# Kernel tuning notes

Hardware: AMD Instinct MI355X
Metric: run time of the kernel (lower is better)

## Reference

```python
import jax, jax.numpy as jnp
import numpy as np

H = 8          # num_heads
NEG = -1e30    # masked-score value
EPS = 1e-5


def layer_norm(h, g, b):
    mu = jnp.mean(h, -1, keepdims=True)
    v = jnp.mean(jnp.square(h - mu), -1, keepdims=True)
    return (h - mu) * jax.lax.rsqrt(v + EPS) * g + b


def mha(q_in, kv_in, in_w, in_b, out_w, out_b, mask):
    # in_w: [3D, D] packed q/k/v projections (PyTorch MultiheadAttention layout)
    D = q_in.shape[-1]
    dh = D // H
    wq, wk, wv = in_w[:D], in_w[D:2 * D], in_w[2 * D:]
    bq, bk, bv = in_b[:D], in_b[D:2 * D], in_b[2 * D:]
    q = (q_in @ wq.T + bq).reshape(q_in.shape[0], q_in.shape[1], H, dh)
    k = (kv_in @ wk.T + bk).reshape(kv_in.shape[0], kv_in.shape[1], H, dh)
    v = (kv_in @ wv.T + bv).reshape(kv_in.shape[0], kv_in.shape[1], H, dh)
    s = jnp.einsum('bqhd,bkhd->bhqk', q, k) / jnp.sqrt(jnp.float32(dh))
    if mask is not None:
        s = s + mask  # [1,1,S,S] additive causal mask
    a = jax.nn.softmax(s, axis=-1)
    o = jnp.einsum('bhqk,bkhd->bqhd', a, v).reshape(q_in.shape[0], q_in.shape[1], D)
    return o @ out_w.T + out_b


def _forward(x, start_query, one_emb, zero_emb,
             sa_in_w, sa_in_b, sa_out_w, sa_out_b,
             ca_in_w, ca_in_b, ca_out_w, ca_out_b,
             lin1_w, lin1_b, lin2_w, lin2_b,
             ln_g, ln_b, cls_w, cls_b, label):
    B, S, D = x.shape
    n = label.shape[0]  # == S
    # Teacher-forced decoder inputs: [start_query, emb(label[0]), ..., emb(label[n-2])]
    tok = jnp.where((label[:-1] > 0.5)[:, None], one_emb[None, :], zero_emb[None, :])  # [n-1, D]
    tgt = jnp.concatenate([start_query[None, :], tok], axis=0)  # [n, D]
    h = jnp.broadcast_to(tgt[None], (B, n, D))
    causal = jnp.tril(jnp.ones((n, n), dtype=bool))
    mask = jnp.where(causal, 0.0, NEG).astype(x.dtype)[None, None]
    L = sa_in_w.shape[0]
    for l in range(L):
        # post-LN TransformerDecoderLayer (PyTorch default, relu FFN)
        sa = mha(h, h, sa_in_w[l], sa_in_b[l], sa_out_w[l], sa_out_b[l], mask)
        h = layer_norm(h + sa, ln_g[l, 0], ln_b[l, 0])
        ca = mha(h, x, ca_in_w[l], ca_in_b[l], ca_out_w[l], ca_out_b[l], None)
        h = layer_norm(h + ca, ln_g[l, 1], ln_b[l, 1])
        ff = jax.nn.relu(h @ lin1_w[l].T + lin1_b[l]) @ lin2_w[l].T + lin2_b[l]
        h = layer_norm(h + ff, ln_g[l, 2], ln_b[l, 2])
    # classifier + sigmoid; output[b, i] == decoder(tf[:1+i])[-1] of the original loop
    return jax.nn.sigmoid(h @ cls_w.T + cls_b)  # [B, n, 1]


def setup_inputs() -> dict:
    key = jax.random.key(0)
    ks = iter(jax.random.split(key, 32))
    B, S, D, FF, L = 8, 1024, 1024, 2048, 6

    def w(shape, s=0.02):
        return jax.random.normal(next(ks), shape, jnp.float32) * s

    return dict(
        x=jax.random.normal(next(ks), (B, S, D), jnp.float32),
        label=jax.random.uniform(next(ks), (S,), jnp.float32),
        start_query=jax.random.uniform(next(ks), (D,), jnp.float32),
        one_emb=jax.random.uniform(next(ks), (D,), jnp.float32),
        zero_emb=jax.random.uniform(next(ks), (D,), jnp.float32),
        sa_in_w=w((L, 3 * D, D)), sa_in_b=jnp.zeros((L, 3 * D), jnp.float32),
        sa_out_w=w((L, D, D)), sa_out_b=jnp.zeros((L, D), jnp.float32),
        ca_in_w=w((L, 3 * D, D)), ca_in_b=jnp.zeros((L, 3 * D), jnp.float32),
        ca_out_w=w((L, D, D)), ca_out_b=jnp.zeros((L, D), jnp.float32),
        lin1_w=w((L, FF, D)), lin1_b=jnp.zeros((L, FF), jnp.float32),
        lin2_w=w((L, D, FF)), lin2_b=jnp.zeros((L, D), jnp.float32),
        ln_g=jnp.ones((L, 3, D), jnp.float32), ln_b=jnp.zeros((L, 3, D), jnp.float32),
        cls_w=w((1, D)), cls_b=jnp.zeros((1,), jnp.float32),
    )


def reference(x, label, start_query, one_emb, zero_emb,
              sa_in_w, sa_in_b, sa_out_w, sa_out_b,
              ca_in_w, ca_in_b, ca_out_w, ca_out_b,
              lin1_w, lin1_b, lin2_w, lin2_b,
              ln_g, ln_b, cls_w, cls_b):
    return _forward(x, start_query, one_emb, zero_emb,
                    sa_in_w, sa_in_b, sa_out_w, sa_out_b,
                    ca_in_w, ca_in_b, ca_out_w, ca_out_b,
                    lin1_w, lin1_b, lin2_w, lin2_b,
                    ln_g, ln_b, cls_w, cls_b, label)
```

## Files before the change

### kernel.cpp

```cpp
#include <hip/hip_runtime.h>
#include <stdint.h>

typedef __attribute__((ext_vector_type(8))) short short8;
typedef __attribute__((ext_vector_type(4))) float f32x4;
typedef __attribute__((ext_vector_type(4))) float float4v;
typedef __attribute__((ext_vector_type(4))) unsigned short ushort4v;

__device__ __forceinline__ float b2f(short u) {
  union { float f; uint32_t i; } v; v.i = ((uint32_t)(unsigned short)u) << 16; return v.f;
}
__device__ __forceinline__ short f2b(float f) {
  uint32_t x = __float_as_uint(f);
  uint32_t r = (x + 0x7fffu + ((x >> 16) & 1u)) >> 16;
  return (short)r;
}
__device__ __forceinline__ void gload16(const short* g, short* l) {
  __builtin_amdgcn_global_load_lds((__attribute__((address_space(1))) const void*)g,
                                   (__attribute__((address_space(3))) void*)l, 16, 0, 0);
}

__global__ void f2b_kernel(const float* __restrict__ in, short* __restrict__ out, int n4) {
  int i = blockIdx.x * blockDim.x + threadIdx.x;
  int stride = gridDim.x * blockDim.x;
  for (; i < n4; i += stride) {
    float4v v = *((const float4v*)in + i);
    ushort4v o;
    o[0] = (unsigned short)f2b(v[0]); o[1] = (unsigned short)f2b(v[1]);
    o[2] = (unsigned short)f2b(v[2]); o[3] = (unsigned short)f2b(v[3]);
    *((ushort4v*)out + i) = o;
  }
}

__global__ void h0_kernel(const float* __restrict__ label, const float* __restrict__ sq,
                          const float* __restrict__ onee, const float* __restrict__ zeroe,
                          short* __restrict__ h) {
  int i = blockIdx.x;
  const float* src = (i == 0) ? sq : (label[i - 1] > 0.5f ? onee : zeroe);
  int d = threadIdx.x * 4;
  float4v v = *(const float4v*)(src + d);
  ushort4v o;
  o[0] = (unsigned short)f2b(v[0]); o[1] = (unsigned short)f2b(v[1]);
  o[2] = (unsigned short)f2b(v[2]); o[3] = (unsigned short)f2b(v[3]);
#pragma unroll
  for (int b = 0; b < 8; ++b)
    *(ushort4v*)(h + ((size_t)b * 1024 + i) * 1024 + d) = o;
}

__device__ __forceinline__ void stage_grp(const short* __restrict__ mat, size_t rc0,
                                          int K, int kt, short* dstbuf, int w, int lane, int g2) {
  const int w3 = w & 3;
  const int rlo = lane >> 3;
  const int us = (lane & 7) ^ rlo;
#pragma unroll
  for (int q = 0; q < 4; ++q) {
    int c;
    if (w < 4) c = g2 * 8 + w3 * 2 + (q & 1) + (q >> 1) * 16;
    else       c = g2 * 4 + w3 + (q & 1) * 8 + (q >> 1) * 16;
    int rih = (c & 15) * 8 + rlo;
    gload16(mat + (rc0 + (c >> 4) * 128 + rih) * (size_t)K + kt * 64 + us * 8,
            dstbuf + ((w >> 2) * 32 + c) * 512);
  }
}

template <int EPI>
__global__ __launch_bounds__(512, 2) void gemm256(const short* __restrict__ A,
                                                  const short* __restrict__ W,
                                                  const float* __restrict__ bias,
                                                  short* __restrict__ C,
                                                  int M, int N, int K) {
  __shared__ short lds[2 * 4 * 8192];
  const int tid = threadIdx.x, lane = tid & 63, w = tid >> 6;
  const int g = lane >> 4, l15 = lane & 15;
  const int wm = w >> 2, wn = w & 3;
  const int nbx = N >> 8;
  int nwg = gridDim.x, orig = blockIdx.x, cpx = nwg >> 3;
  int id = (orig & 7) * cpx + (orig >> 3);
  int bx = id % nbx, by = id / nbx;
  const size_t rowA = (size_t)by * 256, colB = (size_t)bx * 256;
  const int NT = K >> 6;

  const short* smat = (w < 4) ? A : W;
  const size_t src0 = (w < 4) ? rowA : colB;

  f32x4 acc[8][4];
#pragma unroll
  for (int i = 0; i < 8; ++i)
#pragma unroll
    for (int j = 0; j < 4; ++j) acc[i][j] = (f32x4){0.f, 0.f, 0.f, 0.f};

  int sxz0 = g ^ (l15 & 7);
  int sxz1 = (4 + g) ^ (l15 & 7);
  const short* abase = lds + wm * 8192 + l15 * 64;
  const short* bbase = lds + (2 + (wn >> 1)) * 8192 + ((wn & 1) * 64 + l15) * 64;

  stage_grp(smat, src0, K, 0, lds, w, lane, 0);
  stage_grp(smat, src0, K, 0, lds, w, lane, 1);
  asm volatile("s_waitcnt vmcnt(0)" ::: "memory");
  __builtin_amdgcn_s_barrier();

  int p = 0;
  for (int t = 0; t < NT; ++t) {
    const int po = p * 32768;
    short* nbuf = lds + (p ^ 1) * 32768;
    if (t + 1 < NT) stage_grp(smat, src0, K, t + 1, nbuf, w, lane, 0);
    short8 af[4][2], bf0[2][2], bf1[2][2];

#pragma unroll
    for (int i = 0; i < 4; ++i) {
      af[i][0] = *(const short8*)(abase + po + i * 1024 + sxz0 * 8);
      af[i][1] = *(const short8*)(abase + po + i * 1024 + sxz1 * 8);
    }
#pragma unroll
    for (int j = 0; j < 2; ++j) {
      bf0[j][0] = *(const short8*)(bbase + po + j * 1024 + sxz0 * 8);
      bf0[j][1] = *(const short8*)(bbase + po + j * 1024 + sxz1 * 8);
    }
    __builtin_amdgcn_s_barrier();
    __builtin_amdgcn_s_setprio(1);
#pragma unroll
    for (int i = 0; i < 4; ++i)
#pragma unroll
      for (int j = 0; j < 2; ++j)
#pragma unroll
        for (int ks = 0; ks < 2; ++ks)
          acc[i][j] = __builtin_amdgcn_mfma_f32_16x16x32_bf16(af[i][ks], bf0[j][ks], acc[i][j], 0, 0, 0);
    __builtin_amdgcn_s_setprio(0);
    if (t + 1 < NT) {
      asm volatile("s_waitcnt vmcnt(4)" ::: "memory");
      stage_grp(smat, src0, K, t + 1, nbuf, w, lane, 1);
    } else {
      asm volatile("s_waitcnt vmcnt(0)" ::: "memory");
    }
    __builtin_amdgcn_s_barrier();

#pragma unroll
    for (int j = 0; j < 2; ++j) {
      bf1[j][0] = *(const short8*)(bbase + po + (2 + j) * 1024 + sxz0 * 8);
      bf1[j][1] = *(const short8*)(bbase + po + (2 + j) * 1024 + sxz1 * 8);
    }
    __builtin_amdgcn_s_barrier();
    __builtin_amdgcn_s_setprio(1);
#pragma unroll
    for (int i = 0; i < 4; ++i)
#pragma unroll
      for (int j = 0; j < 2; ++j)
#pragma unroll
        for (int ks = 0; ks < 2; ++ks)
          acc[i][2 + j] = __builtin_amdgcn_mfma_f32_16x16x32_bf16(af[i][ks], bf1[j][ks], acc[i][2 + j], 0, 0, 0);
    __builtin_amdgcn_s_setprio(0);
    __builtin_amdgcn_s_barrier();

#pragma unroll
    for (int i = 0; i < 4; ++i) {
      af[i][0] = *(const short8*)(abase + po + (64 + i * 16) * 64 + sxz0 * 8);
      af[i][1] = *(const short8*)(abase + po + (64 + i * 16) * 64 + sxz1 * 8);
    }
    __builtin_amdgcn_s_barrier();
    __builtin_amdgcn_s_setprio(1);
#pragma unroll
    for (int i = 0; i < 4; ++i)
#pragma unroll
      for (int j = 0; j < 2; ++j)
#pragma unroll
        for (int ks = 0; ks < 2; ++ks)
          acc[4 + i][2 + j] = __builtin_amdgcn_mfma_f32_16x16x32_bf16(af[i][ks], bf1[j][ks], acc[4 + i][2 + j], 0, 0, 0);
    __builtin_amdgcn_s_setprio(0);
    __builtin_amdgcn_s_barrier();

    __builtin_amdgcn_s_setprio(1);
#pragma unroll
    for (int i = 0; i < 4; ++i)
#pragma unroll
      for (int j = 0; j < 2; ++j)
#pragma unroll
        for (int ks = 0; ks < 2; ++ks)
          acc[4 + i][j] = __builtin_amdgcn_mfma_f32_16x16x32_bf16(af[i][ks], bf0[j][ks], acc[4 + i][j], 0, 0, 0);
    __builtin_amdgcn_s_setprio(0);

    asm volatile("s_waitcnt vmcnt(4)" ::: "memory");
    __builtin_amdgcn_s_barrier();
    p ^= 1;
  }

  float bv[4];
#pragma unroll
  for (int j = 0; j < 4; ++j) bv[j] = bias[colB + wn * 64 + j * 16 + l15];
#pragma unroll
  for (int i = 0; i < 8; ++i) {
    size_t row = rowA + wm * 128 + i * 16 + g * 4;
#pragma unroll
    for (int j = 0; j < 4; ++j) {
      size_t col = colB + wn * 64 + j * 16 + l15;
#pragma unroll
      for (int r = 0; r < 4; ++r) {
        float v = acc[i][j][r] + bv[j];
        if (EPI == 1) v = fmaxf(v, 0.f);
        C[(row + r) * N + col] = f2b(v);
      }
    }
  }
}

__global__ __launch_bounds__(256) void tv_kernel(const short* __restrict__ src, int ld, int voff,
                                                 short* __restrict__ vt) {
  __shared__ short t[64 * 72];
  const int kt = blockIdx.x * 64, dt = blockIdx.y * 64, bh = blockIdx.z;
  const int b = bh >> 3, hh = bh & 7;
  const short* s = src + (size_t)(b * 1024 + kt) * ld + voff + hh * 128 + dt;
#pragma unroll
  for (int p = 0; p < 2; ++p) {
    int idx = p * 256 + threadIdx.x;
    int r = idx >> 3, u = idx & 7;
    *(short8*)&t[r * 72 + u * 8] = *(const short8*)&s[(size_t)r * ld + u * 8];
  }
  __syncthreads();
#pragma unroll
  for (int p = 0; p < 2; ++p) {
    int idx = p * 256 + threadIdx.x;
    int dd = idx >> 3, u = idx & 7;
    short8 o;
#pragma unroll
    for (int j = 0; j < 8; ++j) o[j] = t[(u * 8 + j) * 72 + dd];
    *(short8*)&vt[((size_t)bh * 128 + dt + dd) * 1024 + kt + u * 8] = o;
  }
}

template <bool CAUSAL>
__global__ __launch_bounds__(256, 2) void attn_kernel(const short* __restrict__ Qb, int ldq, int qoff,
                                                      const short* __restrict__ Kb, int ldk, int koff,
                                                      const short* __restrict__ Vt,
                                                      short* __restrict__ Ob) {
  __shared__ short k_lds[64 * 128];
  __shared__ short v_lds[128 * 64];
  __shared__ short p_lds[4 * 32 * 72];
  const int tid = threadIdx.x, lane = tid & 63, w = tid >> 6;
  const int g = lane >> 4, l15 = lane & 15;
  const int bh = blockIdx.y, b = bh >> 3, hh = bh & 7;
  int qi = blockIdx.x;
  if (CAUSAL) qi = (blockIdx.y & 32) ? 7 - qi : qi;
  const int q0 = qi * 128;
  const float scale = 0.08838834764831845f;

  short8 qf[2][4];
#pragma unroll
  for (int fm = 0; fm < 2; ++fm) {
    int row = q0 + w * 32 + fm * 16 + l15;
    const short* qp = Qb + (size_t)(b * 1024 + row) * ldq + qoff + hh * 128;
#pragma unroll
    for (int t = 0; t < 4; ++t) qf[fm][t] = *(const short8*)(qp + t * 32 + g * 8);
  }

  f32x4 oacc[2][8];
  float m_st[2][4], l_st[2][4];
#pragma unroll
  for (int fm = 0; fm < 2; ++fm) {
#pragma unroll
    for (int fo = 0; fo < 8; ++fo) oacc[fm][fo] = (f32x4){0.f, 0.f, 0.f, 0.f};
#pragma unroll
    for (int r = 0; r < 4; ++r) { m_st[fm][r] = -3.0e38f; l_st[fm][r] = 0.f; }
  }

  const int ktend = CAUSAL ? (q0 >> 6) + 1 : 15;
  for (int kt = 0; kt <= ktend; ++kt) {
    __syncthreads();
#pragma unroll
    for (int c = 0; c < 4; ++c) {
      int ch = w * 4 + c;
      int r = ch * 4 + (lane >> 4);
      int u = lane & 15, us = u ^ (r & 7);
      gload16(Kb + (size_t)(b * 1024 + kt * 64 + r) * ldk + koff + hh * 128 + us * 8,
              (short*)k_lds + ch * 512);
    }
#pragma unroll
    for (int c = 0; c < 4; ++c) {
      int ch = w * 4 + c;
      int d = ch * 8 + (lane >> 3);
      int u = lane & 7, us = u ^ (d & 7);
      gload16(Vt + ((size_t)bh * 128 + d) * 1024 + kt * 64 + us * 8, (short*)v_lds + ch * 512);
    }
    __syncthreads();

    f32x4 sacc[2][4];
#pragma unroll
    for (int fm = 0; fm < 2; ++fm)
#pragma unroll
      for (int fn = 0; fn < 4; ++fn) sacc[fm][fn] = (f32x4){0.f, 0.f, 0.f, 0.f};
#pragma unroll
    for (int t = 0; t < 4; ++t) {
      short8 kf[4];
#pragma unroll
      for (int fn = 0; fn < 4; ++fn) {
        int rowk = fn * 16 + l15;
        int u = (4 * t + g) ^ (rowk & 7);
        kf[fn] = *(const short8*)((const char*)k_lds + rowk * 256 + u * 16);
      }
#pragma unroll
      for (int fm = 0; fm < 2; ++fm)
#pragma unroll
        for (int fn = 0; fn < 4; ++fn)
          sacc[fm][fn] = __builtin_amdgcn_mfma_f32_16x16x32_bf16(qf[fm][t], kf[fn], sacc[fm][fn], 0, 0, 0);
    }

#pragma unroll
    for (int fm = 0; fm < 2; ++fm)
#pragma unroll
      for (int reg = 0; reg < 4; ++reg) {
        float sv[4];
        float mt = -3.0e38f;
#pragma unroll
        for (int fn = 0; fn < 4; ++fn) {
          float s = sacc[fm][fn][reg] * scale;
          if (CAUSAL) {
            int kg = kt * 64 + fn * 16 + l15;
            int qg = q0 + w * 32 + fm * 16 + g * 4 + reg;
            if (kg > qg) s = -1e30f;
          }
          sv[fn] = s;
          mt = fmaxf(mt, s);
        }
#pragma unroll
        for (int off = 1; off < 16; off <<= 1) mt = fmaxf(mt, __shfl_xor(mt, off));
        float mo = m_st[fm][reg];
        float mn = fmaxf(mo, mt);
        float corr = __expf(mo - mn);
        float ps = 0.f;
#pragma unroll
        for (int fn = 0; fn < 4; ++fn) {
          float p = __expf(sv[fn] - mn);
          ps += p;
          p_lds[w * 2304 + (fm * 16 + g * 4 + reg) * 72 + fn * 16 + l15] = f2b(p);
        }
#pragma unroll
        for (int off = 1; off < 16; off <<= 1) ps += __shfl_xor(ps, off);
        l_st[fm][reg] = l_st[fm][reg] * corr + ps;
        m_st[fm][reg] = mn;
#pragma unroll
        for (int fo = 0; fo < 8; ++fo) oacc[fm][fo][reg] *= corr;
      }
    __syncthreads();

#pragma unroll
    for (int t = 0; t < 2; ++t) {
      short8 pf[2];
#pragma unroll
      for (int fm = 0; fm < 2; ++fm)
        pf[fm] = *(const short8*)(p_lds + w * 2304 + (fm * 16 + l15) * 72 + t * 32 + g * 8);
#pragma unroll
      for (int fo = 0; fo < 8; ++fo) {
        int rowd = fo * 16 + l15;
        int u = (4 * t + g) ^ (rowd & 7);
        short8 vf = *(const short8*)((const char*)v_lds + rowd * 128 + u * 16);
#pragma unroll
        for (int fm = 0; fm < 2; ++fm)
          oacc[fm][fo] = __builtin_amdgcn_mfma_f32_16x16x32_bf16(pf[fm], vf, oacc[fm][fo], 0, 0, 0);
      }
    }
  }

#pragma unroll
  for (int fm = 0; fm < 2; ++fm)
#pragma unroll
    for (int fo = 0; fo < 8; ++fo)
#pragma unroll
      for (int reg = 0; reg < 4; ++reg) {
        int row = q0 + w * 32 + fm * 16 + g * 4 + reg;
        int col = hh * 128 + fo * 16 + l15;
        float o = oacc[fm][fo][reg] / l_st[fm][reg];
        Ob[(size_t)(b * 1024 + row) * 1024 + col] = f2b(o);
      }
}

__global__ __launch_bounds__(128) void ln_kernel(const short* __restrict__ h,
                                                 const short* __restrict__ delta,
                                                 const float* __restrict__ gg,
                                                 const float* __restrict__ bb,
                                                 short* __restrict__ out) {
  __shared__ float red[4];
  const int row = blockIdx.x, tid = threadIdx.x;
  const short8 hv = *(const short8*)(h + (size_t)row * 1024 + tid * 8);
  const short8 dv = *(const short8*)(delta + (size_t)row * 1024 + tid * 8);
  float x[8];
  float s = 0.f, s2 = 0.f;
#pragma unroll
  for (int j = 0; j < 8; ++j) {
    x[j] = b2f(hv[j]) + b2f(dv[j]);
    s += x[j];
    s2 += x[j] * x[j];
  }
#pragma unroll
  for (int o = 1; o < 64; o <<= 1) { s += __shfl_xor(s, o); s2 += __shfl_xor(s2, o); }
  if ((tid & 63) == 0) { red[(tid >> 6) * 2] = s; red[(tid >> 6) * 2 + 1] = s2; }
  __syncthreads();
  s = red[0] + red[2];
  s2 = red[1] + red[3];
  const float mu = s * (1.f / 1024.f);
  const float var = s2 * (1.f / 1024.f) - mu * mu;
  const float rs = rsqrtf(var + 1e-5f);
  short8 o;
#pragma unroll
  for (int j = 0; j < 8; ++j) {
    int d = tid * 8 + j;
    o[j] = f2b((x[j] - mu) * rs * gg[d] + bb[d]);
  }
  *(short8*)(out + (size_t)row * 1024 + tid * 8) = o;
}

__global__ __launch_bounds__(256) void cls_kernel(const short* __restrict__ h,
                                                  const float* __restrict__ wv,
                                                  const float* __restrict__ bias,
                                                  float* __restrict__ out) {
  const int lane = threadIdx.x & 63, w = threadIdx.x >> 6;
  const int row = blockIdx.x * 4 + w;
  const short* hp = h + (size_t)row * 1024 + lane * 16;
  float sum = 0.f;
#pragma unroll
  for (int i = 0; i < 2; ++i) {
    short8 v = *(const short8*)(hp + i * 8);
#pragma unroll
    for (int j = 0; j < 8; ++j) sum += b2f(v[j]) * wv[lane * 16 + i * 8 + j];
  }
#pragma unroll
  for (int o = 1; o < 64; o <<= 1) sum += __shfl_xor(sum, o);
  if (lane == 0) {
    float z = sum + bias[0];
    out[row] = 1.f / (1.f + __expf(-z));
  }
}

#define O_SA_IN  ((size_t)0)
#define O_SA_OUT ((size_t)18874368)
#define O_CA_IN  ((size_t)25165824)
#define O_CA_OUT ((size_t)44040192)
#define O_LIN1   ((size_t)50331648)
#define O_LIN2   ((size_t)62914560)
#define O_X      ((size_t)75497472)
#define O_H      ((size_t)83886080)
#define O_QKV    ((size_t)92274688)
#define O_ATTN   ((size_t)117440512)
#define O_DELTA  ((size_t)125829120)
#define O_VT     ((size_t)134217728)
#define O_FF1    ((size_t)142606336)

extern "C" void kernel_launch(void* const* d_in, const int* in_sizes, int n_in,
                              void* d_out, int out_size, void* d_ws, size_t ws_size,
                              hipStream_t stream) {
  const float* x = (const float*)d_in[0];
  const float* label = (const float*)d_in[1];
  const float* sq = (const float*)d_in[2];
  const float* onee = (const float*)d_in[3];
  const float* zeroe = (const float*)d_in[4];
  const float* sa_in_w = (const float*)d_in[5];
  const float* sa_in_b = (const float*)d_in[6];
  const float* sa_out_w = (const float*)d_in[7];
  const float* sa_out_b = (const float*)d_in[8];
  const float* ca_in_w = (const float*)d_in[9];
  const float* ca_in_b = (const float*)d_in[10];
  const float* ca_out_w = (const float*)d_in[11];
  const float* ca_out_b = (const float*)d_in[12];
  const float* lin1_w = (const float*)d_in[13];
  const float* lin1_b = (const float*)d_in[14];
  const float* lin2_w = (const float*)d_in[15];
  const float* lin2_b = (const float*)d_in[16];
  const float* ln_g = (const float*)d_in[17];
  const float* ln_b = (const float*)d_in[18];
  const float* cls_w = (const float*)d_in[19];
  const float* cls_b = (const float*)d_in[20];

  short* ws = (short*)d_ws;
  short* w_sa_in = ws + O_SA_IN;
  short* w_sa_out = ws + O_SA_OUT;
  short* w_ca_in = ws + O_CA_IN;
  short* w_ca_out = ws + O_CA_OUT;
  short* w_lin1 = ws + O_LIN1;
  short* w_lin2 = ws + O_LIN2;
  short* xb = ws + O_X;
  short* hbuf = ws + O_H;
  short* qkv = ws + O_QKV;
  short* kvb = qkv + 8388608;
  short* attnb = ws + O_ATTN;
  short* delta = ws + O_DELTA;
  short* vt = ws + O_VT;
  short* ff1 = ws + O_FF1;

  f2b_kernel<<<4096, 256, 0, stream>>>(sa_in_w, w_sa_in, 18874368 / 4);
  f2b_kernel<<<4096, 256, 0, stream>>>(sa_out_w, w_sa_out, 6291456 / 4);
  f2b_kernel<<<4096, 256, 0, stream>>>(ca_in_w, w_ca_in, 18874368 / 4);
  f2b_kernel<<<4096, 256, 0, stream>>>(ca_out_w, w_ca_out, 6291456 / 4);
  f2b_kernel<<<4096, 256, 0, stream>>>(lin1_w, w_lin1, 12582912 / 4);
  f2b_kernel<<<4096, 256, 0, stream>>>(lin2_w, w_lin2, 12582912 / 4);
  f2b_kernel<<<4096, 256, 0, stream>>>(x, xb, 8388608 / 4);
  h0_kernel<<<1024, 256, 0, stream>>>(label, sq, onee, zeroe, hbuf);

  for (int l = 0; l < 6; ++l) {
    gemm256<0><<<384, 512, 0, stream>>>(hbuf, w_sa_in + (size_t)l * 3145728,
                                        sa_in_b + (size_t)l * 3072, qkv, 8192, 3072, 1024);
    tv_kernel<<<dim3(16, 2, 64), 256, 0, stream>>>(qkv, 3072, 2048, vt);
    attn_kernel<true><<<dim3(8, 64), 256, 0, stream>>>(qkv, 3072, 0, qkv, 3072, 1024, vt, attnb);
    gemm256<0><<<128, 512, 0, stream>>>(attnb, w_sa_out + (size_t)l * 1048576,
                                        sa_out_b + (size_t)l * 1024, delta, 8192, 1024, 1024);
    ln_kernel<<<8192, 128, 0, stream>>>(hbuf, delta, ln_g + (size_t)(l * 3 + 0) * 1024,
                                        ln_b + (size_t)(l * 3 + 0) * 1024, hbuf);
    gemm256<0><<<128, 512, 0, stream>>>(hbuf, w_ca_in + (size_t)l * 3145728,
                                        ca_in_b + (size_t)l * 3072, qkv, 8192, 1024, 1024);
    gemm256<0><<<256, 512, 0, stream>>>(xb, w_ca_in + (size_t)l * 3145728 + 1048576,
                                        ca_in_b + (size_t)l * 3072 + 1024, kvb, 8192, 2048, 1024);
    tv_kernel<<<dim3(16, 2, 64), 256, 0, stream>>>(kvb, 2048, 1024, vt);
    attn_kernel<false><<<dim3(8, 64), 256, 0, stream>>>(qkv, 1024, 0, kvb, 2048, 0, vt, attnb);
    gemm256<0><<<128, 512, 0, stream>>>(attnb, w_ca_out + (size_t)l * 1048576,
                                        ca_out_b + (size_t)l * 1024, delta, 8192, 1024, 1024);
    ln_kernel<<<8192, 128, 0, stream>>>(hbuf, delta, ln_g + (size_t)(l * 3 + 1) * 1024,
                                        ln_b + (size_t)(l * 3 + 1) * 1024, hbuf);
    gemm256<1><<<256, 512, 0, stream>>>(hbuf, w_lin1 + (size_t)l * 2097152,
                                        lin1_b + (size_t)l * 2048, ff1, 8192, 2048, 1024);
    gemm256<0><<<128, 512, 0, stream>>>(ff1, w_lin2 + (size_t)l * 2097152,
                                        lin2_b + (size_t)l * 1024, delta, 8192, 1024, 2048);
    ln_kernel<<<8192, 128, 0, stream>>>(hbuf, delta, ln_g + (size_t)(l * 3 + 2) * 1024,
                                        ln_b + (size_t)(l * 3 + 2) * 1024, hbuf);
  }
  cls_kernel<<<2048, 256, 0, stream>>>(hbuf, cls_w, cls_b, (float*)d_out);
}
```

Before: 2.978 ms.

## Add 256x128-tile GEMM for N=1024 layers and prefetch-pipeline attention K/V tiles

Adds a gemm_n128 kernel with 256x128 tiles, double-buffered LDS and split B staging. It replaces the 256x256 GEMM for the four N=1024 projections, so 256 workgroups launch instead of 128 and fill more of the CUs. The attention kernel now prefetches the next K/V tile into registers while computing the current one, and computes the softmax row sum with an MFMA against a ones vector instead of shuffle reductions. It also raises wave priority around the MFMA sections. The costs are more register pressure and more complex wait-count logic.

```diff
diff --git a/kernel.cpp b/kernel.cpp
--- a/kernel.cpp
+++ b/kernel.cpp
@@ -201,6 +201,134 @@
   }
 }
 
+__device__ __forceinline__ void stage_n128(const short* __restrict__ A, const short* __restrict__ W,
+                                           size_t rowA, size_t colB, int K, int kt,
+                                           short* dstbuf, int w, int lane, int grp) {
+  const int rlo = lane >> 3;
+  const int us = (lane & 7) ^ rlo;
+  const int coff = kt * 64 + us * 8;
+  if (grp == 0) {
+#pragma unroll
+    for (int q = 0; q < 4; ++q) {
+      int c = w * 4 + q;
+      gload16(A + (rowA + (c >> 4) * 128 + (c & 15) * 8 + rlo) * (size_t)K + coff,
+              dstbuf + (c >> 4) * 8192 + (c & 15) * 512 + lane * 8);
+    }
+    int bc = (w & 3) + (w >> 2) * 8;
+    gload16(W + (colB + bc * 8 + rlo) * (size_t)K + coff, dstbuf + 16384 + bc * 512 + lane * 8);
+  } else {
+    int bc = (w & 3) + (w >> 2) * 8 + 4;
+    gload16(W + (colB + bc * 8 + rlo) * (size_t)K + coff, dstbuf + 16384 + bc * 512 + lane * 8);
+  }
+}
+
+template <int EPI>
+__global__ __launch_bounds__(512, 2) void gemm_n128(const short* __restrict__ A,
+                                                    const short* __restrict__ W,
+                                                    const float* __restrict__ bias,
+                                                    short* __restrict__ C,
+                                                    int M, int N, int K) {
+  __shared__ short lds[2 * 24576];
+  const int tid = threadIdx.x, lane = tid & 63, w = tid >> 6;
+  const int g = lane >> 4, l15 = lane & 15;
+  const int wm = w >> 1, wn = w & 1;
+  const int nbx = N >> 7;
+  int nwg = gridDim.x, orig = blockIdx.x, cpx = nwg >> 3;
+  int id = (orig & 7) * cpx + (orig >> 3);
+  int bx = id % nbx, by = id / nbx;
+  const size_t rowA = (size_t)by * 256, colB = (size_t)bx * 128;
+  const int NT = K >> 6;
+
+  f32x4 acc[4][4];
+#pragma unroll
+  for (int i = 0; i < 4; ++i)
+#pragma unroll
+    for (int j = 0; j < 4; ++j) acc[i][j] = (f32x4){0.f, 0.f, 0.f, 0.f};
+
+  const int sxz0 = g ^ (l15 & 7), sxz1 = (4 + g) ^ (l15 & 7);
+  int aoff[4];
+#pragma unroll
+  for (int i = 0; i < 4; ++i) {
+    int ra = wm * 64 + i * 16 + l15;
+    aoff[i] = (ra >> 7) * 8192 + (ra & 127) * 64;
+  }
+  const int boffb = 16384 + (wn * 64 + l15) * 64;
+
+  stage_n128(A, W, rowA, colB, K, 0, lds, w, lane, 0);
+  stage_n128(A, W, rowA, colB, K, 0, lds, w, lane, 1);
+  asm volatile("s_waitcnt vmcnt(0)" ::: "memory");
+  __builtin_amdgcn_s_barrier();
+
+  int p = 0;
+  for (int t = 0; t < NT; ++t) {
+    short* nbuf = lds + (p ^ 1) * 24576;
+    if (t + 1 < NT) stage_n128(A, W, rowA, colB, K, t + 1, nbuf, w, lane, 0);
+    const int po = p * 24576;
+    short8 af[4][2], bf[2][2];
+#pragma unroll
+    for (int i = 0; i < 4; ++i) {
+      af[i][0] = *(const short8*)(lds + po + aoff[i] + sxz0 * 8);
+      af[i][1] = *(const short8*)(lds + po + aoff[i] + sxz1 * 8);
+    }
+#pragma unroll
+    for (int j = 0; j < 2; ++j) {
+      bf[j][0] = *(const short8*)(lds + po + boffb + j * 1024 + sxz0 * 8);
+      bf[j][1] = *(const short8*)(lds + po + boffb + j * 1024 + sxz1 * 8);
+    }
+    __builtin_amdgcn_s_setprio(1);
+#pragma unroll
+    for (int i = 0; i < 4; ++i)
+#pragma unroll
+      for (int j = 0; j < 2; ++j)
+#pragma unroll
+        for (int ks = 0; ks < 2; ++ks)
+          acc[i][j] = __builtin_amdgcn_mfma_f32_16x16x32_bf16(af[i][ks], bf[j][ks], acc[i][j], 0, 0, 0);
+    __builtin_amdgcn_s_setprio(0);
+    if (t + 1 < NT) {
+      asm volatile("s_waitcnt vmcnt(5)" ::: "memory");
+      stage_n128(A, W, rowA, colB, K, t + 1, nbuf, w, lane, 1);
+    } else {
+      asm volatile("s_waitcnt vmcnt(0)" ::: "memory");
+    }
+    __builtin_amdgcn_s_barrier();
+#pragma unroll
+    for (int j = 0; j < 2; ++j) {
+      bf[j][0] = *(const short8*)(lds + po + boffb + 2048 + j * 1024 + sxz0 * 8);
+      bf[j][1] = *(const short8*)(lds + po + boffb + 2048 + j * 1024 + sxz1 * 8);
+    }
+    __builtin_amdgcn_s_setprio(1);
+#pragma unroll
+    for (int i = 0; i < 4; ++i)
+#pragma unroll
+      for (int j = 0; j < 2; ++j)
+#pragma unroll
+        for (int ks = 0; ks < 2; ++ks)
+          acc[i][2 + j] = __builtin_amdgcn_mfma_f32_16x16x32_bf16(af[i][ks], bf[j][ks], acc[i][2 + j], 0, 0, 0);
+    __builtin_amdgcn_s_setprio(0);
+    asm volatile("s_waitcnt vmcnt(1)" ::: "memory");
+    __builtin_amdgcn_s_barrier();
+    p ^= 1;
+  }
+
+  float bv[4];
+#pragma unroll
+  for (int j = 0; j < 4; ++j) bv[j] = bias[colB + wn * 64 + j * 16 + l15];
+#pragma unroll
+  for (int i = 0; i < 4; ++i) {
+    size_t row = rowA + wm * 64 + i * 16 + g * 4;
+#pragma unroll
+    for (int j = 0; j < 4; ++j) {
+      size_t col = colB + wn * 64 + j * 16 + l15;
+#pragma unroll
+      for (int r = 0; r < 4; ++r) {
+        float v = acc[i][j][r] + bv[j];
+        if (EPI == 1) v = fmaxf(v, 0.f);
+        C[(row + r) * N + col] = f2b(v);
+      }
+    }
+  }
+}
+
 __global__ __launch_bounds__(256) void tv_kernel(const short* __restrict__ src, int ld, int voff,
                                                  short* __restrict__ vt) {
   __shared__ short t[64 * 72];
@@ -240,6 +368,10 @@
   if (CAUSAL) qi = (blockIdx.y & 32) ? 7 - qi : qi;
   const int q0 = qi * 128;
   const float scale = 0.08838834764831845f;
+  const int ntiles = CAUSAL ? (q0 >> 6) + 2 : 16;
+
+  const int kr = (w * 4) * 4 + (lane >> 4);
+  const int vd = (w * 4) * 8 + (lane >> 3);
 
   short8 qf[2][4];
 #pragma unroll
@@ -251,35 +383,47 @@
   }
 
   f32x4 oacc[2][8];
-  float m_st[2][4], l_st[2][4];
+  f32x4 lacc[2];
+  float m_st[2][4];
 #pragma unroll
   for (int fm = 0; fm < 2; ++fm) {
 #pragma unroll
     for (int fo = 0; fo < 8; ++fo) oacc[fm][fo] = (f32x4){0.f, 0.f, 0.f, 0.f};
-#pragma unroll
-    for (int r = 0; r < 4; ++r) { m_st[fm][r] = -3.0e38f; l_st[fm][r] = 0.f; }
-  }
-
-  const int ktend = CAUSAL ? (q0 >> 6) + 1 : 15;
-  for (int kt = 0; kt <= ktend; ++kt) {
-    __syncthreads();
+    lacc[fm] = (f32x4){0.f, 0.f, 0.f, 0.f};
+#pragma unroll
+    for (int r = 0; r < 4; ++r) m_st[fm][r] = -3.0e38f;
+  }
+  const short8 ones = {16256, 16256, 16256, 16256, 16256, 16256, 16256, 16256};
+
+#pragma unroll
+  for (int c = 0; c < 4; ++c) {
+    int ch = w * 4 + c;
+    int r = kr + c * 4;
+    int us = (lane & 15) ^ (r & 7);
+    gload16(Kb + (size_t)(b * 1024 + r) * ldk + koff + hh * 128 + us * 8, k_lds + ch * 512);
+    int d = vd + c * 8;
+    int usv = (lane & 7) ^ (d & 7);
+    gload16(Vt + ((size_t)bh * 128 + d) * 1024 + usv * 8, v_lds + ch * 512);
+  }
+  __builtin_amdgcn_sched_barrier(0);
+  short8 kreg[4], vreg[4];
+  if (ntiles > 1) {
 #pragma unroll
     for (int c = 0; c < 4; ++c) {
-      int ch = w * 4 + c;
-      int r = ch * 4 + (lane >> 4);
-      int u = lane & 15, us = u ^ (r & 7);
-      gload16(Kb + (size_t)(b * 1024 + kt * 64 + r) * ldk + koff + hh * 128 + us * 8,
-              (short*)k_lds + ch * 512);
-    }
-#pragma unroll
-    for (int c = 0; c < 4; ++c) {
-      int ch = w * 4 + c;
-      int d = ch * 8 + (lane >> 3);
-      int u = lane & 7, us = u ^ (d & 7);
-      gload16(Vt + ((size_t)bh * 128 + d) * 1024 + kt * 64 + us * 8, (short*)v_lds + ch * 512);
-    }
-    __syncthreads();
-
+      int r = kr + c * 4;
+      int us = (lane & 15) ^ (r & 7);
+      kreg[c] = *(const short8*)(Kb + (size_t)(b * 1024 + 64 + r) * ldk + koff + hh * 128 + us * 8);
+      int d = vd + c * 8;
+      int usv = (lane & 7) ^ (d & 7);
+      vreg[c] = *(const short8*)(Vt + ((size_t)bh * 128 + d) * 1024 + 64 + usv * 8);
+    }
+    asm volatile("s_waitcnt vmcnt(8)" ::: "memory");
+  } else {
+    asm volatile("s_waitcnt vmcnt(0)" ::: "memory");
+  }
+  __builtin_amdgcn_s_barrier();
+
+  for (int kt = 0; kt < ntiles; ++kt) {
     f32x4 sacc[2][4];
 #pragma unroll
     for (int fm = 0; fm < 2; ++fm)
@@ -294,11 +438,13 @@
         int u = (4 * t + g) ^ (rowk & 7);
         kf[fn] = *(const short8*)((const char*)k_lds + rowk * 256 + u * 16);
       }
+      __builtin_amdgcn_s_setprio(1);
 #pragma unroll
       for (int fm = 0; fm < 2; ++fm)
 #pragma unroll
         for (int fn = 0; fn < 4; ++fn)
           sacc[fm][fn] = __builtin_amdgcn_mfma_f32_16x16x32_bf16(qf[fm][t], kf[fn], sacc[fm][fn], 0, 0, 0);
+      __builtin_amdgcn_s_setprio(0);
     }
 
 #pragma unroll
@@ -323,21 +469,16 @@
         float mo = m_st[fm][reg];
         float mn = fmaxf(mo, mt);
         float corr = __expf(mo - mn);
-        float ps = 0.f;
 #pragma unroll
         for (int fn = 0; fn < 4; ++fn) {
           float p = __expf(sv[fn] - mn);
-          ps += p;
           p_lds[w * 2304 + (fm * 16 + g * 4 + reg) * 72 + fn * 16 + l15] = f2b(p);
         }
-#pragma unroll
-        for (int off = 1; off < 16; off <<= 1) ps += __shfl_xor(ps, off);
-        l_st[fm][reg] = l_st[fm][reg] * corr + ps;
         m_st[fm][reg] = mn;
+        lacc[fm][reg] *= corr;
 #pragma unroll
         for (int fo = 0; fo < 8; ++fo) oacc[fm][fo][reg] *= corr;
       }
-    __syncthreads();
 
 #pragma unroll
     for (int t = 0; t < 2; ++t) {
@@ -345,15 +486,45 @@
 #pragma unroll
       for (int fm = 0; fm < 2; ++fm)
         pf[fm] = *(const short8*)(p_lds + w * 2304 + (fm * 16 + l15) * 72 + t * 32 + g * 8);
+      __builtin_amdgcn_s_setprio(1);
+      lacc[0] = __builtin_amdgcn_mfma_f32_16x16x32_bf16(pf[0], ones, lacc[0], 0, 0, 0);
+      lacc[1] = __builtin_amdgcn_mfma_f32_16x16x32_bf16(pf[1], ones, lacc[1], 0, 0, 0);
+      __builtin_amdgcn_s_setprio(0);
 #pragma unroll
       for (int fo = 0; fo < 8; ++fo) {
         int rowd = fo * 16 + l15;
         int u = (4 * t + g) ^ (rowd & 7);
         short8 vf = *(const short8*)((const char*)v_lds + rowd * 128 + u * 16);
+        __builtin_amdgcn_s_setprio(1);
 #pragma unroll
         for (int fm = 0; fm < 2; ++fm)
           oacc[fm][fo] = __builtin_amdgcn_mfma_f32_16x16x32_bf16(pf[fm], vf, oacc[fm][fo], 0, 0, 0);
-      }
+        __builtin_amdgcn_s_setprio(0);
+      }
+    }
+
+    if (kt + 1 < ntiles) {
+      __builtin_amdgcn_s_barrier();
+      asm volatile("s_waitcnt vmcnt(0)" ::: "memory");
+#pragma unroll
+      for (int c = 0; c < 4; ++c) {
+        int ch = w * 4 + c;
+        *(short8*)(k_lds + ch * 512 + lane * 8) = kreg[c];
+        *(short8*)(v_lds + ch * 512 + lane * 8) = vreg[c];
+      }
+      if (kt + 2 < ntiles) {
+#pragma unroll
+        for (int c = 0; c < 4; ++c) {
+          int r = kr + c * 4;
+          int us = (lane & 15) ^ (r & 7);
+          kreg[c] = *(const short8*)(Kb + (size_t)(b * 1024 + (kt + 2) * 64 + r) * ldk + koff + hh * 128 + us * 8);
+          int d = vd + c * 8;
+          int usv = (lane & 7) ^ (d & 7);
+          vreg[c] = *(const short8*)(Vt + ((size_t)bh * 128 + d) * 1024 + (kt + 2) * 64 + usv * 8);
+        }
+      }
+      asm volatile("s_waitcnt lgkmcnt(0)" ::: "memory");
+      __builtin_amdgcn_s_barrier();
     }
   }
 
@@ -365,7 +536,7 @@
       for (int reg = 0; reg < 4; ++reg) {
         int row = q0 + w * 32 + fm * 16 + g * 4 + reg;
         int col = hh * 128 + fo * 16 + l15;
-        float o = oacc[fm][fo][reg] / l_st[fm][reg];
+        float o = oacc[fm][fo][reg] / lacc[fm][reg];
         Ob[(size_t)(b * 1024 + row) * 1024 + col] = f2b(o);
       }
 }
@@ -496,24 +667,24 @@
                                         sa_in_b + (size_t)l * 3072, qkv, 8192, 3072, 1024);
     tv_kernel<<<dim3(16, 2, 64), 256, 0, stream>>>(qkv, 3072, 2048, vt);
     attn_kernel<true><<<dim3(8, 64), 256, 0, stream>>>(qkv, 3072, 0, qkv, 3072, 1024, vt, attnb);
-    gemm256<0><<<128, 512, 0, stream>>>(attnb, w_sa_out + (size_t)l * 1048576,
-                                        sa_out_b + (size_t)l * 1024, delta, 8192, 1024, 1024);
+    gemm_n128<0><<<256, 512, 0, stream>>>(attnb, w_sa_out + (size_t)l * 1048576,
+                                          sa_out_b + (size_t)l * 1024, delta, 8192, 1024, 1024);
     ln_kernel<<<8192, 128, 0, stream>>>(hbuf, delta, ln_g + (size_t)(l * 3 + 0) * 1024,
                                         ln_b + (size_t)(l * 3 + 0) * 1024, hbuf);
-    gemm256<0><<<128, 512, 0, stream>>>(hbuf, w_ca_in + (size_t)l * 3145728,
-                                        ca_in_b + (size_t)l * 3072, qkv, 8192, 1024, 1024);
+    gemm_n128<0><<<256, 512, 0, stream>>>(hbuf, w_ca_in + (size_t)l * 3145728,
+                                          ca_in_b + (size_t)l * 3072, qkv, 8192, 1024, 1024);
     gemm256<0><<<256, 512, 0, stream>>>(xb, w_ca_in + (size_t)l * 3145728 + 1048576,
                                         ca_in_b + (size_t)l * 3072 + 1024, kvb, 8192, 2048, 1024);
     tv_kernel<<<dim3(16, 2, 64), 256, 0, stream>>>(kvb, 2048, 1024, vt);
     attn_kernel<false><<<dim3(8, 64), 256, 0, stream>>>(qkv, 1024, 0, kvb, 2048, 0, vt, attnb);
-    gemm256<0><<<128, 512, 0, stream>>>(attnb, w_ca_out + (size_t)l * 1048576,
-                                        ca_out_b + (size_t)l * 1024, delta, 8192, 1024, 1024);
+    gemm_n128<0><<<256, 512, 0, stream>>>(attnb, w_ca_out + (size_t)l * 1048576,
+                                          ca_out_b + (size_t)l * 1024, delta, 8192, 1024, 1024);
     ln_kernel<<<8192, 128, 0, stream>>>(hbuf, delta, ln_g + (size_t)(l * 3 + 1) * 1024,
                                         ln_b + (size_t)(l * 3 + 1) * 1024, hbuf);
     gemm256<1><<<256, 512, 0, stream>>>(hbuf, w_lin1 + (size_t)l * 2097152,
                                         lin1_b + (size_t)l * 2048, ff1, 8192, 2048, 1024);
-    gemm256<0><<<128, 512, 0, stream>>>(ff1, w_lin2 + (size_t)l * 2097152,
-                                        lin2_b + (size_t)l * 1024, delta, 8192, 1024, 2048);
+    gemm_n128<0><<<256, 512, 0, stream>>>(ff1, w_lin2 + (size_t)l * 2097152,
+                                          lin2_b + (size_t)l * 1024, delta, 8192, 1024, 2048);
     ln_kernel<<<8192, 128, 0, stream>>>(hbuf, delta, ln_g + (size_t)(l * 3 + 2) * 1024,
                                         ln_b + (size_t)(l * 3 + 2) * 1024, hbuf);
   }
```

New measurement: 2.680 ms. -10.0%, faster.
